# Kernel optimization log

Hardware: AMD Instinct MI355X
Metric: run time of the kernel (lower is better)

Reference implementation:

```python
import jax, jax.numpy as jnp
import numpy as np

TEMPERATURE = 8.0  # sqrt(d_head=64)
NEG_INF = -1e15


def setup_inputs() -> dict:
    key = jax.random.key(0)
    k1, k2_, k3, k4, k5, k6 = jax.random.split(key, 6)
    BH, N, D = 16, 2048, 64
    B = 2  # edge batch; BH // B == 8 heads
    return {
        "q": jax.random.normal(k1, (BH, N, D), dtype=jnp.float32),
        "k": jax.random.normal(k2_, (BH, N, D), dtype=jnp.float32),
        "v": jax.random.normal(k3, (BH, N, D), dtype=jnp.float32),
        "k2": jax.random.normal(k4, (BH, N, D), dtype=jnp.float32),
        "mask": jax.random.randint(k5, (BH, 1, N), 0, 2) > 0,
        "edge": jax.random.randint(k6, (B, N, N), 0, 2).astype(jnp.int32),
    }


def reference(q, k, v, k2, mask, edge):
    # attn scores: [bh, n, m]
    attn = jnp.einsum("bnd,bmd->bnm", q, k) / TEMPERATURE
    # torch .repeat along dim0 == tile
    reps = attn.shape[0] // edge.shape[0]
    edge_t = jnp.tile(edge, (reps, 1, 1))
    attn = jnp.where(edge_t == 0, NEG_INF, attn)
    attn = jnp.where(mask, NEG_INF, attn)
    attn = jax.nn.softmax(attn, axis=2)  # dropout p=0 (eval)
    output = jnp.einsum("bnm,bmd->bnd", attn, v)
    # non_linear=False, so no sigmoid
    return (output, attn)
```

## Files before the change

### kernel.cpp

```cpp
#include <hip/hip_runtime.h>
#include <stdint.h>
#include <math.h>

#define BH_ 16
#define N_  2048
#define D_  64
#define NEGV (-1e15f)

typedef __attribute__((ext_vector_type(8))) short bf16x8;
typedef __attribute__((ext_vector_type(8))) unsigned short us8;
typedef __attribute__((ext_vector_type(4))) float f32x4;

#define OFF_MASKU8 0u
#define OFF_MBITS  32768u
#define OFF_EBITS  65536u
#define OFF_QBF    1114112u
#define OFF_KBF    5308416u
#define OFF_VT     9502720u
#define WS_V6      13697024u
#define OFF_PSUM   13697024u
#define OFF_OPART  14221312u
#define WS_V7      30998528u

#define BARRIER_LGKM() do {                                   \
    asm volatile("s_waitcnt lgkmcnt(0)" ::: "memory");        \
    __builtin_amdgcn_sched_barrier(0);                        \
    __builtin_amdgcn_s_barrier();                             \
    __builtin_amdgcn_sched_barrier(0);                        \
} while (0)

__device__ __forceinline__ unsigned short f2bf(float f) {
    unsigned u = __float_as_uint(f);
    return (unsigned short)((u + 0x7FFFu + ((u >> 16) & 1u)) >> 16);
}

__global__ __launch_bounds__(256)
void prep_all(const float* __restrict__ q, const float* __restrict__ k,
              const float* __restrict__ v, const void* __restrict__ mraw,
              const int* __restrict__ edge,
              unsigned short* __restrict__ qbf, unsigned short* __restrict__ kbf,
              unsigned short* __restrict__ vT,
              unsigned short* __restrict__ e16, unsigned long long* __restrict__ mbits)
{
    __shared__ unsigned short shbuf[64][72];
    __shared__ int flag;
    const int bid = blockIdx.x;
    const int t   = threadIdx.x;

    if (bid < 2048) {
        const int idx = bid * 256 + t;
        const int4* p = (const int4*)(edge + (size_t)idx * 16);
        unsigned m = 0;
        #pragma unroll
        for (int i = 0; i < 4; ++i) {
            const int4 vv = p[i];
            m |= (vv.x != 0 ? 1u : 0u) << (i * 4 + 0);
            m |= (vv.y != 0 ? 1u : 0u) << (i * 4 + 1);
            m |= (vv.z != 0 ? 1u : 0u) << (i * 4 + 2);
            m |= (vv.w != 0 ? 1u : 0u) << (i * 4 + 3);
        }
        e16[idx] = (unsigned short)m;
    } else if (bid < 2560) {
        const int b2 = bid - 2048;
        const int rt = b2 & 31, bh = b2 >> 5;
        const size_t base = ((size_t)bh * N_ + (size_t)rt * 64) * D_;
        #pragma unroll
        for (int i = 0; i < 4; ++i) {
            const int idx = t + i * 256;
            float4 f = *(const float4*)(q + base + (size_t)idx * 4);
            ushort4 s; s.x = f2bf(f.x); s.y = f2bf(f.y); s.z = f2bf(f.z); s.w = f2bf(f.w);
            *(ushort4*)(qbf + base + (size_t)idx * 4) = s;
            f = *(const float4*)(k + base + (size_t)idx * 4);
            s.x = f2bf(f.x); s.y = f2bf(f.y); s.z = f2bf(f.z); s.w = f2bf(f.w);
            *(ushort4*)(kbf + base + (size_t)idx * 4) = s;
            f = *(const float4*)(v + base + (size_t)idx * 4);
            const int row = idx >> 4;
            const int d0  = (idx & 15) * 4;
            shbuf[d0 + 0][row] = f2bf(f.x);
            shbuf[d0 + 1][row] = f2bf(f.y);
            shbuf[d0 + 2][row] = f2bf(f.z);
            shbuf[d0 + 3][row] = f2bf(f.w);
        }
        __syncthreads();
        const int d  = t >> 2;
        const int c4 = (t & 3) * 16;
        const size_t ob = ((size_t)bh * D_ + d) * N_ + (size_t)rt * 64 + c4;
        *(us8*)(vT + ob)     = *(us8*)&shbuf[d][c4];
        *(us8*)(vT + ob + 8) = *(us8*)&shbuf[d][c4 + 8];
    } else {
        const int bh = bid - 2560;
        if (t == 0) flag = 0;
        __syncthreads();
        const int* mi = (const int*)mraw;
        int bad = 0;
        for (int i = t; i < 8192; i += 256)
            if ((unsigned)mi[i] > 1u) bad = 1;
        if (bad) atomicOr(&flag, 1);
        __syncthreads();
        const int is_u8 = flag;
        const uint8_t* m8 = (const uint8_t*)mraw;
        const int w4 = t >> 6, l = t & 63;
        for (int it = 0; it < 8; ++it) {
            const int pos = bh * 2048 + it * 256 + w4 * 64 + l;
            const bool on = is_u8 ? (m8[pos] != 0) : (mi[pos] != 0);
            unsigned long long bal = __ballot(on);
            if (l == 0) mbits[bh * 32 + it * 4 + w4] = bal;
        }
    }
}

__global__ __launch_bounds__(256)
void attn_sumk(const unsigned short* __restrict__ qbf,
               const unsigned short* __restrict__ kbf,
               const unsigned long long* __restrict__ ebits,
               const unsigned long long* __restrict__ mbits,
               float* __restrict__ psum)
{
    __shared__ unsigned short sK[2][4096];

    const int tile = blockIdx.x, bh = blockIdx.y, s = blockIdx.z;
    const int t = threadIdx.x;
    const int w = t >> 6, lane = t & 63, l15 = lane & 15, lg = lane >> 4;
    const int rbase = tile * 64;
    const int myrow = rbase + w * 16 + l15;
    const int kcb = s * 8;

    const unsigned short* qb = qbf + (size_t)bh * N_ * D_;
    const unsigned short* kb = kbf + (size_t)bh * N_ * D_;
    const unsigned long long* ebrow =
        ebits + ((size_t)(bh & 1) * N_ + (size_t)myrow) * 32;
    const unsigned long long* mb = mbits + bh * 32;

    const bf16x8 aq0 = *(const bf16x8*)(qb + (size_t)myrow * D_ + lg * 8);
    const bf16x8 aq1 = *(const bf16x8*)(qb + (size_t)myrow * D_ + lg * 8 + 32);

    const int s0row = t >> 3, s1row = s0row + 32, t8 = t & 7;
    const int ds0 = s0row * 64 + ((t8 ^ (s0row & 7)) * 8);
    const int ds1 = s1row * 64 + ((t8 ^ (s1row & 7)) * 8);

    {
        const unsigned short* src = kb + (size_t)kcb * 4096;
        *(us8*)(sK[0] + ds0) = *(const us8*)(src + (size_t)t * 8);
        *(us8*)(sK[0] + ds1) = *(const us8*)(src + (size_t)(t + 256) * 8);
        BARRIER_LGKM();
    }
    float lacc = 0.f;
    #pragma unroll 1
    for (int i = 0; i < 8; ++i) {
        const int kc = kcb + i;
        const int cur = i & 1;
        us8 nk0, nk1;
        if (i < 7) {
            const unsigned short* src = kb + (size_t)(kc + 1) * 4096;
            nk0 = *(const us8*)(src + (size_t)t * 8);
            nk1 = *(const us8*)(src + (size_t)(t + 256) * 8);
        }
        const unsigned long long wbits = ebrow[kc] & ~mb[kc];
        const unsigned short* kcur = sK[cur];
        #pragma unroll
        for (int nt = 0; nt < 4; ++nt) {
            const int row = nt * 16 + l15, sw = row & 7;
            const bf16x8 k0 = *(const bf16x8*)(kcur + row * 64 + ((lg ^ sw) * 8));
            const bf16x8 k1 = *(const bf16x8*)(kcur + row * 64 + (((lg + 4) ^ sw) * 8));
            f32x4 c = (f32x4){0.f, 0.f, 0.f, 0.f};
            c = __builtin_amdgcn_mfma_f32_16x16x32_bf16(k0, aq0, c, 0, 0, 0);
            c = __builtin_amdgcn_mfma_f32_16x16x32_bf16(k1, aq1, c, 0, 0, 0);
            const unsigned bits = (unsigned)(wbits >> (nt * 16 + lg * 4)) & 0xFu;
            #pragma unroll
            for (int r = 0; r < 4; ++r)
                lacc += ((bits >> r) & 1u) ? __expf(c[r] * 0.125f) : 0.f;
        }
        if (i < 7) {
            *(us8*)(sK[cur ^ 1] + ds0) = nk0;
            *(us8*)(sK[cur ^ 1] + ds1) = nk1;
        }
        BARRIER_LGKM();
    }
    lacc += __shfl_xor(lacc, 16);
    lacc += __shfl_xor(lacc, 32);
    if (lane < 16) psum[((size_t)bh * N_ + myrow) * 4 + s] = lacc;
}

__global__ __launch_bounds__(256)
void attn_pvk(const unsigned short* __restrict__ qbf,
              const unsigned short* __restrict__ kbf,
              const unsigned short* __restrict__ vT,
              const unsigned long long* __restrict__ ebits,
              const unsigned long long* __restrict__ mbits,
              const float* __restrict__ psum,
              float* __restrict__ opart, float* __restrict__ attn)
{
    __shared__ unsigned short sK[2][4096];
    __shared__ unsigned short sV[2][4096];
    __shared__ char pbuf[4][2048];

    const int tile = blockIdx.x, bh = blockIdx.y, s = blockIdx.z;
    const int t = threadIdx.x;
    const int w = t >> 6, lane = t & 63, l15 = lane & 15, lg = lane >> 4;
    const int rbase = tile * 64;
    const int myrow = rbase + w * 16 + l15;
    const int kcb = s * 16;

    const unsigned short* qb = qbf + (size_t)bh * N_ * D_;
    const unsigned short* kb = kbf + (size_t)bh * N_ * D_;
    const unsigned short* vb = vT  + (size_t)bh * D_ * N_;
    const unsigned long long* ebrow =
        ebits + ((size_t)(bh & 1) * N_ + (size_t)myrow) * 32;
    const unsigned long long* mb = mbits + bh * 32;
    float* arow = attn + (size_t)bh * N_ * N_ + (size_t)myrow * N_ + lg * 4;

    const f32x4 ps = *(const f32x4*)(psum + ((size_t)bh * N_ + myrow) * 4);
    const float inv = 1.0f / (ps[0] + ps[1] + ps[2] + ps[3]);

    const bf16x8 aq0 = *(const bf16x8*)(qb + (size_t)myrow * D_ + lg * 8);
    const bf16x8 aq1 = *(const bf16x8*)(qb + (size_t)myrow * D_ + lg * 8 + 32);

    const int s0row = t >> 3, s1row = s0row + 32, t8 = t & 7;
    const int ds0 = s0row * 64 + ((t8 ^ (s0row & 7)) * 8);
    const int ds1 = s1row * 64 + ((t8 ^ (s1row & 7)) * 8);

    {
        const unsigned short* srck = kb + (size_t)kcb * 4096;
        const unsigned short* srcv = vb + (size_t)kcb * 64;
        *(us8*)(sK[0] + ds0) = *(const us8*)(srck + (size_t)t * 8);
        *(us8*)(sK[0] + ds1) = *(const us8*)(srck + (size_t)(t + 256) * 8);
        *(us8*)(sV[0] + ds0) = *(const us8*)(srcv + (size_t)s0row * 2048 + t8 * 8);
        *(us8*)(sV[0] + ds1) = *(const us8*)(srcv + (size_t)s1row * 2048 + t8 * 8);
        BARRIER_LGKM();
    }

    f32x4 o[4];
    #pragma unroll
    for (int nt = 0; nt < 4; ++nt) o[nt] = (f32x4){0.f, 0.f, 0.f, 0.f};

    char* pbw = pbuf[w];
    const int swzP = (l15 & 7) << 4;
    const int ab0 = (l15 * 128 + lg * 16)      ^ swzP;
    const int ab1 = (l15 * 128 + lg * 16 + 64) ^ swzP;

    #pragma unroll 1
    for (int i = 0; i < 16; ++i) {
        const int kc = kcb + i;
        const int cur = i & 1;
        us8 nk0, nk1, nv0, nv1;
        if (i < 15) {
            const unsigned short* srck = kb + (size_t)(kc + 1) * 4096;
            const unsigned short* srcv = vb + (size_t)(kc + 1) * 64;
            nk0 = *(const us8*)(srck + (size_t)t * 8);
            nk1 = *(const us8*)(srck + (size_t)(t + 256) * 8);
            nv0 = *(const us8*)(srcv + (size_t)s0row * 2048 + t8 * 8);
            nv1 = *(const us8*)(srcv + (size_t)s1row * 2048 + t8 * 8);
        }
        const unsigned long long wbits = ebrow[kc] & ~mb[kc];
        const unsigned short* kcur = sK[cur];
        float4 ev[4];
        #pragma unroll
        for (int nt = 0; nt < 4; ++nt) {
            const int row = nt * 16 + l15, sw = row & 7;
            const bf16x8 k0 = *(const bf16x8*)(kcur + row * 64 + ((lg ^ sw) * 8));
            const bf16x8 k1 = *(const bf16x8*)(kcur + row * 64 + (((lg + 4) ^ sw) * 8));
            f32x4 c = (f32x4){0.f, 0.f, 0.f, 0.f};
            c = __builtin_amdgcn_mfma_f32_16x16x32_bf16(k0, aq0, c, 0, 0, 0);
            c = __builtin_amdgcn_mfma_f32_16x16x32_bf16(k1, aq1, c, 0, 0, 0);
            const unsigned bits = (unsigned)(wbits >> (nt * 16 + lg * 4)) & 0xFu;
            float4 e;
            e.x = (bits & 1u) ? __expf(c[0] * 0.125f) * inv : 0.f;
            e.y = (bits & 2u) ? __expf(c[1] * 0.125f) * inv : 0.f;
            e.z = (bits & 4u) ? __expf(c[2] * 0.125f) * inv : 0.f;
            e.w = (bits & 8u) ? __expf(c[3] * 0.125f) * inv : 0.f;
            ev[nt] = e;
            ushort4 pe;
            pe.x = f2bf(e.x); pe.y = f2bf(e.y); pe.z = f2bf(e.z); pe.w = f2bf(e.w);
            const int wbyte = (l15 * 128 + nt * 32 + lg * 8) ^ swzP;
            *(ushort4*)(pbw + wbyte) = pe;
        }
        const bf16x8 ap0 = *(const bf16x8*)(pbw + ab0);
        const bf16x8 ap1 = *(const bf16x8*)(pbw + ab1);
        const unsigned short* vcur = sV[cur];
        #pragma unroll
        for (int nt = 0; nt < 4; ++nt) {
            const int row = nt * 16 + l15, sw = row & 7;
            const bf16x8 bv0 = *(const bf16x8*)(vcur + row * 64 + ((lg ^ sw) * 8));
            const bf16x8 bv1 = *(const bf16x8*)(vcur + row * 64 + (((lg + 4) ^ sw) * 8));
            o[nt] = __builtin_amdgcn_mfma_f32_16x16x32_bf16(ap0, bv0, o[nt], 0, 0, 0);
            o[nt] = __builtin_amdgcn_mfma_f32_16x16x32_bf16(ap1, bv1, o[nt], 0, 0, 0);
        }
        {
            float* astore = arow + kc * 64;
            #pragma unroll
            for (int nt = 0; nt < 4; ++nt)
                *(float4*)(astore + nt * 16) = ev[nt];
        }
        if (i < 15) {
            *(us8*)(sK[cur ^ 1] + ds0) = nk0;
            *(us8*)(sK[cur ^ 1] + ds1) = nk1;
            *(us8*)(sV[cur ^ 1] + ds0) = nv0;
            *(us8*)(sV[cur ^ 1] + ds1) = nv1;
        }
        BARRIER_LGKM();
    }

    float* op = opart + (size_t)s * (BH_ * N_ * D_) + (size_t)bh * N_ * D_;
    #pragma unroll
    for (int nt = 0; nt < 4; ++nt)
        #pragma unroll
        for (int r = 0; r < 4; ++r)
            op[(size_t)(rbase + w * 16 + lg * 4 + r) * D_ + nt * 16 + l15] = o[nt][r];
}

__global__ __launch_bounds__(256)
void reduce_o(const float* __restrict__ opart, float* __restrict__ out)
{
    const float4* a = (const float4*)opart;
    const float4* b = a + 524288;
    float4* o4 = (float4*)out;
    const size_t i = (size_t)blockIdx.x * 256 + threadIdx.x;
    float4 x = a[i], y = b[i];
    o4[i] = make_float4(x.x + y.x, x.y + y.y, x.z + y.z, x.w + y.w);
    const size_t j = i + 262144;
    x = a[j]; y = b[j];
    o4[j] = make_float4(x.x + y.x, x.y + y.y, x.z + y.z, x.w + y.w);
}

__global__ __launch_bounds__(256)
void attn_v6(const unsigned short* __restrict__ qbf,
             const unsigned short* __restrict__ kbf,
             const unsigned short* __restrict__ vT,
             const unsigned long long* __restrict__ ebits,
             const unsigned long long* __restrict__ mbits,
             float* __restrict__ out, float* __restrict__ attn)
{
    __shared__ unsigned short sK[2][4096];
    __shared__ unsigned short sV[2][4096];
    __shared__ char pbuf[4][2048];

    const int tile = blockIdx.x;
    const int bh   = blockIdx.y;
    const int t    = threadIdx.x;
    const int w    = t >> 6;
    const int lane = t & 63;
    const int l15  = lane & 15;
    const int lg   = lane >> 4;
    const int rbase = tile * 64;
    const int myrow = rbase + w * 16 + l15;

    const unsigned short* qb = qbf + (size_t)bh * N_ * D_;
    const unsigned short* kb = kbf + (size_t)bh * N_ * D_;
    const unsigned short* vb = vT  + (size_t)bh * D_ * N_;
    const unsigned long long* ebrow =
        ebits + ((size_t)(bh & 1) * N_ + (size_t)myrow) * 32;
    const unsigned long long* mb = mbits + bh * 32;
    float* outb = out + (size_t)bh * N_ * D_;
    float* arow = attn + (size_t)bh * N_ * N_ + (size_t)myrow * N_ + lg * 4;

    const bf16x8 aq0 = *(const bf16x8*)(qb + (size_t)myrow * D_ + lg * 8);
    const bf16x8 aq1 = *(const bf16x8*)(qb + (size_t)myrow * D_ + lg * 8 + 32);

    const int s0row = t >> 3;
    const int s1row = s0row + 32;
    const int t8    = t & 7;
    const int ds0 = s0row * 64 + ((t8 ^ (s0row & 7)) * 8);
    const int ds1 = s1row * 64 + ((t8 ^ (s1row & 7)) * 8);

    {
        const us8 a0 = *(const us8*)(kb + (size_t)t * 8);
        const us8 a1 = *(const us8*)(kb + (size_t)(t + 256) * 8);
        *(us8*)(sK[0] + ds0) = a0;
        *(us8*)(sK[0] + ds1) = a1;
        BARRIER_LGKM();
    }
    float lacc = 0.f;
    #pragma unroll 1
    for (int kc = 0; kc < 32; ++kc) {
        const int cur = kc & 1;
        us8 nk0, nk1;
        if (kc < 31) {
            const unsigned short* s = kb + (size_t)(kc + 1) * 4096;
            nk0 = *(const us8*)(s + (size_t)t * 8);
            nk1 = *(const us8*)(s + (size_t)(t + 256) * 8);
        }
        const unsigned long long wbits = ebrow[kc] & ~mb[kc];
        const unsigned short* kcur = sK[cur];
        #pragma unroll
        for (int nt = 0; nt < 4; ++nt) {
            const int row = nt * 16 + l15, sw = row & 7;
            const bf16x8 k0 = *(const bf16x8*)(kcur + row * 64 + ((lg ^ sw) * 8));
            const bf16x8 k1 = *(const bf16x8*)(kcur + row * 64 + (((lg + 4) ^ sw) * 8));
            f32x4 c = (f32x4){0.f, 0.f, 0.f, 0.f};
            c = __builtin_amdgcn_mfma_f32_16x16x32_bf16(k0, aq0, c, 0, 0, 0);
            c = __builtin_amdgcn_mfma_f32_16x16x32_bf16(k1, aq1, c, 0, 0, 0);
            const unsigned bits = (unsigned)(wbits >> (nt * 16 + lg * 4)) & 0xFu;
            #pragma unroll
            for (int r = 0; r < 4; ++r)
                lacc += ((bits >> r) & 1u) ? __expf(c[r] * 0.125f) : 0.f;
        }
        if (kc < 31) {
            *(us8*)(sK[cur ^ 1] + ds0) = nk0;
            *(us8*)(sK[cur ^ 1] + ds1) = nk1;
        }
        BARRIER_LGKM();
    }
    lacc += __shfl_xor(lacc, 16);
    lacc += __shfl_xor(lacc, 32);
    const float inv = 1.0f / lacc;

    {
        const us8 a0 = *(const us8*)(kb + (size_t)t * 8);
        const us8 a1 = *(const us8*)(kb + (size_t)(t + 256) * 8);
        const us8 b0 = *(const us8*)(vb + (size_t)s0row * 2048 + t8 * 8);
        const us8 b1 = *(const us8*)(vb + (size_t)s1row * 2048 + t8 * 8);
        *(us8*)(sK[0] + ds0) = a0;
        *(us8*)(sK[0] + ds1) = a1;
        *(us8*)(sV[0] + ds0) = b0;
        *(us8*)(sV[0] + ds1) = b1;
        BARRIER_LGKM();
    }

    f32x4 o[4];
    #pragma unroll
    for (int nt = 0; nt < 4; ++nt) o[nt] = (f32x4){0.f, 0.f, 0.f, 0.f};

    char* pbw = pbuf[w];
    const int swzP = (l15 & 7) << 4;
    const int ab0 = (l15 * 128 + lg * 16)      ^ swzP;
    const int ab1 = (l15 * 128 + lg * 16 + 64) ^ swzP;

    #pragma unroll 1
    for (int kc = 0; kc < 32; ++kc) {
        const int cur = kc & 1;
        us8 nk0, nk1, nv0, nv1;
        if (kc < 31) {
            const unsigned short* srck = kb + (size_t)(kc + 1) * 4096;
            const unsigned short* srcv = vb + (size_t)(kc + 1) * 64;
            nk0 = *(const us8*)(srck + (size_t)t * 8);
            nk1 = *(const us8*)(srck + (size_t)(t + 256) * 8);
            nv0 = *(const us8*)(srcv + (size_t)s0row * 2048 + t8 * 8);
            nv1 = *(const us8*)(srcv + (size_t)s1row * 2048 + t8 * 8);
        }
        const unsigned long long wbits = ebrow[kc] & ~mb[kc];
        const unsigned short* kcur = sK[cur];
        float4 ev[4];
        #pragma unroll
        for (int nt = 0; nt < 4; ++nt) {
            const int row = nt * 16 + l15, sw = row & 7;
            const bf16x8 k0 = *(const bf16x8*)(kcur + row * 64 + ((lg ^ sw) * 8));
            const bf16x8 k1 = *(const bf16x8*)(kcur + row * 64 + (((lg + 4) ^ sw) * 8));
            f32x4 c = (f32x4){0.f, 0.f, 0.f, 0.f};
            c = __builtin_amdgcn_mfma_f32_16x16x32_bf16(k0, aq0, c, 0, 0, 0);
            c = __builtin_amdgcn_mfma_f32_16x16x32_bf16(k1, aq1, c, 0, 0, 0);
            const unsigned bits = (unsigned)(wbits >> (nt * 16 + lg * 4)) & 0xFu;
            float4 e;
            e.x = (bits & 1u) ? __expf(c[0] * 0.125f) * inv : 0.f;
            e.y = (bits & 2u) ? __expf(c[1] * 0.125f) * inv : 0.f;
            e.z = (bits & 4u) ? __expf(c[2] * 0.125f) * inv : 0.f;
            e.w = (bits & 8u) ? __expf(c[3] * 0.125f) * inv : 0.f;
            ev[nt] = e;
            ushort4 pe;
            pe.x = f2bf(e.x); pe.y = f2bf(e.y); pe.z = f2bf(e.z); pe.w = f2bf(e.w);
            const int wbyte = (l15 * 128 + nt * 32 + lg * 8) ^ swzP;
            *(ushort4*)(pbw + wbyte) = pe;
        }
        const bf16x8 ap0 = *(const bf16x8*)(pbw + ab0);
        const bf16x8 ap1 = *(const bf16x8*)(pbw + ab1);
        const unsigned short* vcur = sV[cur];
        #pragma unroll
        for (int nt = 0; nt < 4; ++nt) {
            const int row = nt * 16 + l15, sw = row & 7;
            const bf16x8 bv0 = *(const bf16x8*)(vcur + row * 64 + ((lg ^ sw) * 8));
            const bf16x8 bv1 = *(const bf16x8*)(vcur + row * 64 + (((lg + 4) ^ sw) * 8));
            o[nt] = __builtin_amdgcn_mfma_f32_16x16x32_bf16(ap0, bv0, o[nt], 0, 0, 0);
            o[nt] = __builtin_amdgcn_mfma_f32_16x16x32_bf16(ap1, bv1, o[nt], 0, 0, 0);
        }
        {
            float* astore = arow + kc * 64;
            #pragma unroll
            for (int nt = 0; nt < 4; ++nt)
                *(float4*)(astore + nt * 16) = ev[nt];
        }
        if (kc < 31) {
            *(us8*)(sK[cur ^ 1] + ds0) = nk0;
            *(us8*)(sK[cur ^ 1] + ds1) = nk1;
            *(us8*)(sV[cur ^ 1] + ds0) = nv0;
            *(us8*)(sV[cur ^ 1] + ds1) = nv1;
        }
        BARRIER_LGKM();
    }

    #pragma unroll
    for (int nt = 0; nt < 4; ++nt)
        #pragma unroll
        for (int r = 0; r < 4; ++r)
            outb[(size_t)(rbase + w * 16 + lg * 4 + r) * D_ + nt * 16 + l15] = o[nt][r];
}

__global__ __launch_bounds__(256)
void normalize_mask(const void* __restrict__ mask_raw, uint8_t* __restrict__ mask_out)
{
    __shared__ int is_u8;
    const int t = threadIdx.x;
    if (t == 0) is_u8 = 0;
    __syncthreads();
    const int* mi = (const int*)mask_raw;
    int bad = 0;
    for (int i = t; i < 8192; i += 256)
        if ((unsigned)mi[i] > 1u) bad = 1;
    if (bad) atomicOr(&is_u8, 1);
    __syncthreads();
    const int total = BH_ * N_;
    if (is_u8) {
        const uint8_t* m8 = (const uint8_t*)mask_raw;
        for (int i = t; i < total; i += 256) mask_out[i] = m8[i] ? 1 : 0;
    } else {
        for (int i = t; i < total; i += 256) mask_out[i] = (uint8_t)mi[i];
    }
}

__global__ __launch_bounds__(256)
void attn_fused(const float* __restrict__ q, const float* __restrict__ k,
                const float* __restrict__ v, const uint8_t* __restrict__ mask,
                const int* __restrict__ edge, float* __restrict__ out,
                float* __restrict__ attn)
{
    __shared__ float qsT[D_][64 + 4];
    __shared__ float kt [D_][64 + 4];
    __shared__ float vs [64][D_ + 4];
    const int tile = blockIdx.x, bh = blockIdx.y, t = threadIdx.x;
    const int rg = t >> 4, cg = t & 15, r0 = rg * 4, c0 = cg * 4;
    const int row_base = tile * 64;
    const float* qb = q + (size_t)bh * N_ * D_;
    const float* kb = k + (size_t)bh * N_ * D_;
    const float* vb = v + (size_t)bh * N_ * D_;
    const uint8_t* mbp = mask + (size_t)bh * N_;
    const int* ebp = edge + (size_t)(bh & 1) * N_ * N_;
    float* outb = out + (size_t)bh * N_ * D_;
    float* attnb = attn + (size_t)bh * N_ * N_;
    {
        const int rr = t >> 2, dblk = (t & 3) * 16;
        const float* src = qb + (size_t)(row_base + rr) * D_ + dblk;
        #pragma unroll
        for (int qq = 0; qq < 4; ++qq) {
            float4 val = *(const float4*)(src + qq * 4);
            qsT[dblk + qq*4 + 0][rr] = val.x; qsT[dblk + qq*4 + 1][rr] = val.y;
            qsT[dblk + qq*4 + 2][rr] = val.z; qsT[dblk + qq*4 + 3][rr] = val.w;
        }
    }
    float m_i[4], l_i[4];
    #pragma unroll
    for (int i = 0; i < 4; ++i) { m_i[i] = -INFINITY; l_i[i] = 0.f; }
    for (int kc = 0; kc < 32; ++kc) {
        __syncthreads();
        {
            const int ccr = t >> 2, dblk = (t & 3) * 16;
            const float* src = kb + (size_t)(kc * 64 + ccr) * D_ + dblk;
            #pragma unroll
            for (int qq = 0; qq < 4; ++qq) {
                float4 val = *(const float4*)(src + qq * 4);
                kt[dblk + qq*4 + 0][ccr] = val.x; kt[dblk + qq*4 + 1][ccr] = val.y;
                kt[dblk + qq*4 + 2][ccr] = val.z; kt[dblk + qq*4 + 3][ccr] = val.w;
            }
        }
        __syncthreads();
        float sc[4][4];
        #pragma unroll
        for (int i = 0; i < 4; ++i) { sc[i][0]=sc[i][1]=sc[i][2]=sc[i][3]=0.f; }
        for (int d = 0; d < D_; ++d) {
            const float4 qv = *(const float4*)&qsT[d][r0];
            const float4 kv = *(const float4*)&kt[d][c0];
            #pragma unroll
            for (int i = 0; i < 4; ++i) {
                const float qi = (i==0)?qv.x:(i==1)?qv.y:(i==2)?qv.z:qv.w;
                sc[i][0] = fmaf(qi, kv.x, sc[i][0]); sc[i][1] = fmaf(qi, kv.y, sc[i][1]);
                sc[i][2] = fmaf(qi, kv.z, sc[i][2]); sc[i][3] = fmaf(qi, kv.w, sc[i][3]);
            }
        }
        const int cbase = kc * 64 + c0;
        const uint8_t m0 = mbp[cbase], m1 = mbp[cbase+1], m2 = mbp[cbase+2], m3 = mbp[cbase+3];
        #pragma unroll
        for (int i = 0; i < 4; ++i) {
            const int rglob = row_base + r0 + i;
            const int4 e4 = *(const int4*)(ebp + (size_t)rglob * N_ + cbase);
            float s0 = sc[i][0]*0.125f, s1 = sc[i][1]*0.125f, s2 = sc[i][2]*0.125f, s3 = sc[i][3]*0.125f;
            if (e4.x == 0 || m0) s0 = NEGV; if (e4.y == 0 || m1) s1 = NEGV;
            if (e4.z == 0 || m2) s2 = NEGV; if (e4.w == 0 || m3) s3 = NEGV;
            float cmax = fmaxf(fmaxf(s0,s1), fmaxf(s2,s3));
            cmax = fmaxf(cmax, __shfl_xor(cmax,1)); cmax = fmaxf(cmax, __shfl_xor(cmax,2));
            cmax = fmaxf(cmax, __shfl_xor(cmax,4)); cmax = fmaxf(cmax, __shfl_xor(cmax,8));
            const float nm = fmaxf(m_i[i], cmax);
            float ss = __expf(s0-nm)+__expf(s1-nm)+__expf(s2-nm)+__expf(s3-nm);
            ss += __shfl_xor(ss,1); ss += __shfl_xor(ss,2); ss += __shfl_xor(ss,4); ss += __shfl_xor(ss,8);
            l_i[i] = l_i[i]*__expf(m_i[i]-nm) + ss; m_i[i] = nm;
        }
    }
    float inv_l[4];
    #pragma unroll
    for (int i = 0; i < 4; ++i) inv_l[i] = 1.0f / l_i[i];
    float oacc[4][4];
    #pragma unroll
    for (int i = 0; i < 4; ++i) { oacc[i][0]=oacc[i][1]=oacc[i][2]=oacc[i][3]=0.f; }
    for (int kc = 0; kc < 32; ++kc) {
        __syncthreads();
        {
            const int ccr = t >> 2, dblk = (t & 3) * 16;
            const float* src = kb + (size_t)(kc * 64 + ccr) * D_ + dblk;
            #pragma unroll
            for (int qq = 0; qq < 4; ++qq) {
                float4 val = *(const float4*)(src + qq * 4);
                kt[dblk + qq*4 + 0][ccr] = val.x; kt[dblk + qq*4 + 1][ccr] = val.y;
                kt[dblk + qq*4 + 2][ccr] = val.z; kt[dblk + qq*4 + 3][ccr] = val.w;
            }
            const float* srcv = vb + (size_t)(kc * 64 + ccr) * D_ + dblk;
            #pragma unroll
            for (int qq = 0; qq < 4; ++qq)
                *(float4*)&vs[ccr][dblk + qq * 4] = *(const float4*)(srcv + qq * 4);
        }
        __syncthreads();
        float sc[4][4];
        #pragma unroll
        for (int i = 0; i < 4; ++i) { sc[i][0]=sc[i][1]=sc[i][2]=sc[i][3]=0.f; }
        for (int d = 0; d < D_; ++d) {
            const float4 qv = *(const float4*)&qsT[d][r0];
            const float4 kv = *(const float4*)&kt[d][c0];
            #pragma unroll
            for (int i = 0; i < 4; ++i) {
                const float qi = (i==0)?qv.x:(i==1)?qv.y:(i==2)?qv.z:qv.w;
                sc[i][0] = fmaf(qi, kv.x, sc[i][0]); sc[i][1] = fmaf(qi, kv.y, sc[i][1]);
                sc[i][2] = fmaf(qi, kv.z, sc[i][2]); sc[i][3] = fmaf(qi, kv.w, sc[i][3]);
            }
        }
        const int cbase = kc * 64 + c0;
        const uint8_t m0 = mbp[cbase], m1 = mbp[cbase+1], m2 = mbp[cbase+2], m3 = mbp[cbase+3];
        float p[4][4];
        #pragma unroll
        for (int i = 0; i < 4; ++i) {
            const int rglob = row_base + r0 + i;
            const int4 e4 = *(const int4*)(ebp + (size_t)rglob * N_ + cbase);
            float s0 = sc[i][0]*0.125f, s1 = sc[i][1]*0.125f, s2 = sc[i][2]*0.125f, s3 = sc[i][3]*0.125f;
            if (e4.x == 0 || m0) s0 = NEGV; if (e4.y == 0 || m1) s1 = NEGV;
            if (e4.z == 0 || m2) s2 = NEGV; if (e4.w == 0 || m3) s3 = NEGV;
            p[i][0] = __expf(s0-m_i[i])*inv_l[i]; p[i][1] = __expf(s1-m_i[i])*inv_l[i];
            p[i][2] = __expf(s2-m_i[i])*inv_l[i]; p[i][3] = __expf(s3-m_i[i])*inv_l[i];
            *(float4*)&attnb[(size_t)rglob * N_ + cbase] = make_float4(p[i][0],p[i][1],p[i][2],p[i][3]);
        }
        __syncthreads();
        #pragma unroll
        for (int i = 0; i < 4; ++i)
            *(float4*)&kt[r0 + i][c0] = make_float4(p[i][0],p[i][1],p[i][2],p[i][3]);
        __syncthreads();
        for (int c4 = 0; c4 < 64; c4 += 4) {
            float prr[4][4];
            #pragma unroll
            for (int i = 0; i < 4; ++i) {
                const float4 tmp = *(const float4*)&kt[r0 + i][c4];
                prr[i][0]=tmp.x; prr[i][1]=tmp.y; prr[i][2]=tmp.z; prr[i][3]=tmp.w;
            }
            #pragma unroll
            for (int cc = 0; cc < 4; ++cc) {
                const float4 vv = *(const float4*)&vs[c4 + cc][c0];
                #pragma unroll
                for (int i = 0; i < 4; ++i) {
                    oacc[i][0] = fmaf(prr[i][cc], vv.x, oacc[i][0]);
                    oacc[i][1] = fmaf(prr[i][cc], vv.y, oacc[i][1]);
                    oacc[i][2] = fmaf(prr[i][cc], vv.z, oacc[i][2]);
                    oacc[i][3] = fmaf(prr[i][cc], vv.w, oacc[i][3]);
                }
            }
        }
    }
    #pragma unroll
    for (int i = 0; i < 4; ++i)
        *(float4*)&outb[(size_t)(row_base + r0 + i) * D_ + c0] =
            make_float4(oacc[i][0], oacc[i][1], oacc[i][2], oacc[i][3]);
}

extern "C" void kernel_launch(void* const* d_in, const int* in_sizes, int n_in,
                              void* d_out, int out_size, void* d_ws, size_t ws_size,
                              hipStream_t stream) {
    const float* q    = (const float*)d_in[0];
    const float* k    = (const float*)d_in[1];
    const float* v    = (const float*)d_in[2];
    const void*  mraw = d_in[4];
    const int*   edge = (const int*)d_in[5];

    float* out  = (float*)d_out;
    float* attn = (float*)d_out + (size_t)BH_ * N_ * D_;

    char* ws = (char*)d_ws;

    if (ws_size < (size_t)WS_V6) {
        uint8_t* mask_u8 = (uint8_t*)(ws + OFF_MASKU8);
        normalize_mask<<<1, 256, 0, stream>>>(mraw, mask_u8);
        attn_fused<<<dim3(32, 16), 256, 0, stream>>>(q, k, v, mask_u8, edge, out, attn);
        return;
    }

    unsigned long long* mbits = (unsigned long long*)(ws + OFF_MBITS);
    unsigned short*     e16   = (unsigned short*)(ws + OFF_EBITS);
    unsigned short*     qbf   = (unsigned short*)(ws + OFF_QBF);
    unsigned short*     kbf   = (unsigned short*)(ws + OFF_KBF);
    unsigned short*     vT    = (unsigned short*)(ws + OFF_VT);

    prep_all<<<dim3(2576), 256, 0, stream>>>(q, k, v, mraw, edge,
                                             qbf, kbf, vT, e16, mbits);

    if (ws_size >= (size_t)WS_V7) {
        float* psum  = (float*)(ws + OFF_PSUM);
        float* opart = (float*)(ws + OFF_OPART);
        attn_sumk<<<dim3(32, 16, 4), 256, 0, stream>>>(
            qbf, kbf, (const unsigned long long*)e16, mbits, psum);
        attn_pvk<<<dim3(32, 16, 2), 256, 0, stream>>>(
            qbf, kbf, vT, (const unsigned long long*)e16, mbits, psum, opart, attn);
        reduce_o<<<dim3(1024), 256, 0, stream>>>(opart, out);
    } else {
        attn_v6<<<dim3(N_ / 64, BH_), 256, 0, stream>>>(
            qbf, kbf, vT, (const unsigned long long*)e16, mbits, out, attn);
    }
}
```

Before: 136.0 us.

## Drop key-split in PV kernel, write output directly, reorder grid to bh-major

The PV pass no longer splits the key dimension across two blocks. Each block now loops over all 32 key chunks and writes the final output directly, which removes the partial-output buffer and the separate reduce kernel. The grid axes are also swapped so consecutive blocks cover different heads, which changes scheduling and L2 locality for K/V and the edge bits. In exchange the PV grid has half as many blocks (512 instead of 1024), so there is less parallelism to hide latency, while the extra launch and the partial write and read traffic are gone.

```diff
diff --git a/kernel.cpp b/kernel.cpp
--- a/kernel.cpp
+++ b/kernel.cpp
@@ -19,8 +19,7 @@
 #define OFF_VT     9502720u
 #define WS_V6      13697024u
 #define OFF_PSUM   13697024u
-#define OFF_OPART  14221312u
-#define WS_V7      30998528u
+#define WS_V11     14221312u
 
 #define BARRIER_LGKM() do {                                   \
     asm volatile("s_waitcnt lgkmcnt(0)" ::: "memory");        \
@@ -118,7 +117,7 @@
 {
     __shared__ unsigned short sK[2][4096];
 
-    const int tile = blockIdx.x, bh = blockIdx.y, s = blockIdx.z;
+    const int bh = blockIdx.x, tile = blockIdx.y, s = blockIdx.z;
     const int t = threadIdx.x;
     const int w = t >> 6, lane = t & 63, l15 = lane & 15, lg = lane >> 4;
     const int rbase = tile * 64;
@@ -182,24 +181,27 @@
 }
 
 __global__ __launch_bounds__(256)
-void attn_pvk(const unsigned short* __restrict__ qbf,
+void attn_pv2(const unsigned short* __restrict__ qbf,
               const unsigned short* __restrict__ kbf,
               const unsigned short* __restrict__ vT,
               const unsigned long long* __restrict__ ebits,
               const unsigned long long* __restrict__ mbits,
               const float* __restrict__ psum,
-              float* __restrict__ opart, float* __restrict__ attn)
+              float* __restrict__ out, float* __restrict__ attn)
 {
     __shared__ unsigned short sK[2][4096];
     __shared__ unsigned short sV[2][4096];
     __shared__ char pbuf[4][2048];
 
-    const int tile = blockIdx.x, bh = blockIdx.y, s = blockIdx.z;
-    const int t = threadIdx.x;
-    const int w = t >> 6, lane = t & 63, l15 = lane & 15, lg = lane >> 4;
+    const int bh   = blockIdx.x;
+    const int tile = blockIdx.y;
+    const int t    = threadIdx.x;
+    const int w    = t >> 6;
+    const int lane = t & 63;
+    const int l15  = lane & 15;
+    const int lg   = lane >> 4;
     const int rbase = tile * 64;
     const int myrow = rbase + w * 16 + l15;
-    const int kcb = s * 16;
 
     const unsigned short* qb = qbf + (size_t)bh * N_ * D_;
     const unsigned short* kb = kbf + (size_t)bh * N_ * D_;
@@ -207,6 +209,7 @@
     const unsigned long long* ebrow =
         ebits + ((size_t)(bh & 1) * N_ + (size_t)myrow) * 32;
     const unsigned long long* mb = mbits + bh * 32;
+    float* outb = out + (size_t)bh * N_ * D_;
     float* arow = attn + (size_t)bh * N_ * N_ + (size_t)myrow * N_ + lg * 4;
 
     const f32x4 ps = *(const f32x4*)(psum + ((size_t)bh * N_ + myrow) * 4);
@@ -215,17 +218,17 @@
     const bf16x8 aq0 = *(const bf16x8*)(qb + (size_t)myrow * D_ + lg * 8);
     const bf16x8 aq1 = *(const bf16x8*)(qb + (size_t)myrow * D_ + lg * 8 + 32);
 
-    const int s0row = t >> 3, s1row = s0row + 32, t8 = t & 7;
+    const int s0row = t >> 3;
+    const int s1row = s0row + 32;
+    const int t8    = t & 7;
     const int ds0 = s0row * 64 + ((t8 ^ (s0row & 7)) * 8);
     const int ds1 = s1row * 64 + ((t8 ^ (s1row & 7)) * 8);
 
     {
-        const unsigned short* srck = kb + (size_t)kcb * 4096;
-        const unsigned short* srcv = vb + (size_t)kcb * 64;
-        *(us8*)(sK[0] + ds0) = *(const us8*)(srck + (size_t)t * 8);
-        *(us8*)(sK[0] + ds1) = *(const us8*)(srck + (size_t)(t + 256) * 8);
-        *(us8*)(sV[0] + ds0) = *(const us8*)(srcv + (size_t)s0row * 2048 + t8 * 8);
-        *(us8*)(sV[0] + ds1) = *(const us8*)(srcv + (size_t)s1row * 2048 + t8 * 8);
+        *(us8*)(sK[0] + ds0) = *(const us8*)(kb + (size_t)t * 8);
+        *(us8*)(sK[0] + ds1) = *(const us8*)(kb + (size_t)(t + 256) * 8);
+        *(us8*)(sV[0] + ds0) = *(const us8*)(vb + (size_t)s0row * 2048 + t8 * 8);
+        *(us8*)(sV[0] + ds1) = *(const us8*)(vb + (size_t)s1row * 2048 + t8 * 8);
         BARRIER_LGKM();
     }
 
@@ -239,11 +242,10 @@
     const int ab1 = (l15 * 128 + lg * 16 + 64) ^ swzP;
 
     #pragma unroll 1
-    for (int i = 0; i < 16; ++i) {
-        const int kc = kcb + i;
-        const int cur = i & 1;
+    for (int kc = 0; kc < 32; ++kc) {
+        const int cur = kc & 1;
         us8 nk0, nk1, nv0, nv1;
-        if (i < 15) {
+        if (kc < 31) {
             const unsigned short* srck = kb + (size_t)(kc + 1) * 4096;
             const unsigned short* srcv = vb + (size_t)(kc + 1) * 64;
             nk0 = *(const us8*)(srck + (size_t)t * 8);
@@ -291,7 +293,7 @@
             for (int nt = 0; nt < 4; ++nt)
                 *(float4*)(astore + nt * 16) = ev[nt];
         }
-        if (i < 15) {
+        if (kc < 31) {
             *(us8*)(sK[cur ^ 1] + ds0) = nk0;
             *(us8*)(sK[cur ^ 1] + ds1) = nk1;
             *(us8*)(sV[cur ^ 1] + ds0) = nv0;
@@ -300,30 +302,15 @@
         BARRIER_LGKM();
     }
 
-    float* op = opart + (size_t)s * (BH_ * N_ * D_) + (size_t)bh * N_ * D_;
     #pragma unroll
     for (int nt = 0; nt < 4; ++nt)
         #pragma unroll
         for (int r = 0; r < 4; ++r)
-            op[(size_t)(rbase + w * 16 + lg * 4 + r) * D_ + nt * 16 + l15] = o[nt][r];
+            outb[(size_t)(rbase + w * 16 + lg * 4 + r) * D_ + nt * 16 + l15] = o[nt][r];
 }
 
 __global__ __launch_bounds__(256)
-void reduce_o(const float* __restrict__ opart, float* __restrict__ out)
-{
-    const float4* a = (const float4*)opart;
-    const float4* b = a + 524288;
-    float4* o4 = (float4*)out;
-    const size_t i = (size_t)blockIdx.x * 256 + threadIdx.x;
-    float4 x = a[i], y = b[i];
-    o4[i] = make_float4(x.x + y.x, x.y + y.y, x.z + y.z, x.w + y.w);
-    const size_t j = i + 262144;
-    x = a[j]; y = b[j];
-    o4[j] = make_float4(x.x + y.x, x.y + y.y, x.z + y.z, x.w + y.w);
-}
-
-__global__ __launch_bounds__(256)
-void attn_v6(const unsigned short* __restrict__ qbf,
+void attn_v8(const unsigned short* __restrict__ qbf,
              const unsigned short* __restrict__ kbf,
              const unsigned short* __restrict__ vT,
              const unsigned long long* __restrict__ ebits,
@@ -334,8 +321,8 @@
     __shared__ unsigned short sV[2][4096];
     __shared__ char pbuf[4][2048];
 
-    const int tile = blockIdx.x;
-    const int bh   = blockIdx.y;
+    const int bh   = blockIdx.x;
+    const int tile = blockIdx.y;
     const int t    = threadIdx.x;
     const int w    = t >> 6;
     const int lane = t & 63;
@@ -363,10 +350,8 @@
     const int ds1 = s1row * 64 + ((t8 ^ (s1row & 7)) * 8);
 
     {
-        const us8 a0 = *(const us8*)(kb + (size_t)t * 8);
-        const us8 a1 = *(const us8*)(kb + (size_t)(t + 256) * 8);
-        *(us8*)(sK[0] + ds0) = a0;
-        *(us8*)(sK[0] + ds1) = a1;
+        *(us8*)(sK[0] + ds0) = *(const us8*)(kb + (size_t)t * 8);
+        *(us8*)(sK[0] + ds1) = *(const us8*)(kb + (size_t)(t + 256) * 8);
         BARRIER_LGKM();
     }
     float lacc = 0.f;
@@ -405,14 +390,10 @@
     const float inv = 1.0f / lacc;
 
     {
-        const us8 a0 = *(const us8*)(kb + (size_t)t * 8);
-        const us8 a1 = *(const us8*)(kb + (size_t)(t + 256) * 8);
-        const us8 b0 = *(const us8*)(vb + (size_t)s0row * 2048 + t8 * 8);
-        const us8 b1 = *(const us8*)(vb + (size_t)s1row * 2048 + t8 * 8);
-        *(us8*)(sK[0] + ds0) = a0;
-        *(us8*)(sK[0] + ds1) = a1;
-        *(us8*)(sV[0] + ds0) = b0;
-        *(us8*)(sV[0] + ds1) = b1;
+        *(us8*)(sK[0] + ds0) = *(const us8*)(kb + (size_t)t * 8);
+        *(us8*)(sK[0] + ds1) = *(const us8*)(kb + (size_t)(t + 256) * 8);
+        *(us8*)(sV[0] + ds0) = *(const us8*)(vb + (size_t)s0row * 2048 + t8 * 8);
+        *(us8*)(sV[0] + ds1) = *(const us8*)(vb + (size_t)s1row * 2048 + t8 * 8);
         BARRIER_LGKM();
     }
 
@@ -702,16 +683,14 @@
     prep_all<<<dim3(2576), 256, 0, stream>>>(q, k, v, mraw, edge,
                                              qbf, kbf, vT, e16, mbits);
 
-    if (ws_size >= (size_t)WS_V7) {
-        float* psum  = (float*)(ws + OFF_PSUM);
-        float* opart = (float*)(ws + OFF_OPART);
-        attn_sumk<<<dim3(32, 16, 4), 256, 0, stream>>>(
+    if (ws_size >= (size_t)WS_V11) {
+        float* psum = (float*)(ws + OFF_PSUM);
+        attn_sumk<<<dim3(BH_, 32, 4), 256, 0, stream>>>(
             qbf, kbf, (const unsigned long long*)e16, mbits, psum);
-        attn_pvk<<<dim3(32, 16, 2), 256, 0, stream>>>(
-            qbf, kbf, vT, (const unsigned long long*)e16, mbits, psum, opart, attn);
-        reduce_o<<<dim3(1024), 256, 0, stream>>>(opart, out);
+        attn_pv2<<<dim3(BH_, 32), 256, 0, stream>>>(
+            qbf, kbf, vT, (const unsigned long long*)e16, mbits, psum, out, attn);
     } else {
-        attn_v6<<<dim3(N_ / 64, BH_), 256, 0, stream>>>(
+        attn_v8<<<dim3(BH_, N_ / 64), 256, 0, stream>>>(
             qbf, kbf, vT, (const unsigned long long*)e16, mbits, out, attn);
     }
 }
```

New measurement: 125.8 us. 7.5% less time.
